# Kernel optimization log

Measured on AMD Instinct MI355X. Metric: run time of the kernel, lower is better.

The kernel has to match this reference:

```python
import jax, jax.numpy as jnp
import numpy as np

DIM = 2048
HEADS = 32
WINDOW = 8   # local_attn
B = 4
N = 197


def _local_mask(w, n):
    # Faithful to local_attention(): for row i, columns j in [max(i-w,0), min(i+w, n))
    # get weight (w - |i-j|/2)/w; everything else is 0 (later masked to -inf).
    i = jnp.arange(n)[:, None]
    j = jnp.arange(n)[None, :]
    d = jnp.abs(i - j).astype(jnp.float32)
    in_win = (j >= i - w) & (j < i + w)  # range(start, end) excludes i+w
    return jnp.where(in_win, (w - d / 2.0) / w, 0.0)  # (N, N)


def setup_inputs() -> dict:
    key = jax.random.key(0)
    k1, k2, k3, k4 = jax.random.split(key, 4)
    x = jax.random.normal(k1, (B, N, DIM), dtype=jnp.float32)
    qkv_w = jax.random.normal(k2, (3 * DIM, DIM), dtype=jnp.float32) * 0.02  # no qkv bias
    proj_w = jax.random.normal(k3, (DIM, DIM), dtype=jnp.float32) * 0.02
    proj_b = jax.random.normal(k4, (DIM,), dtype=jnp.float32) * 0.02
    return {"x": x, "qkv_w": qkv_w, "proj_w": proj_w, "proj_b": proj_b}


def reference(x, qkv_w, proj_w, proj_b):
    Bb, Nn, C = x.shape
    H = HEADS
    hd = C // H
    scale = hd ** (-0.5)
    # qkv projection: (B, N, 3C) -> (3, B, H, N, hd)
    qkv = (x @ qkv_w.T).reshape(Bb, Nn, 3, H, hd).transpose(2, 0, 3, 1, 4)
    q, k, v = qkv[0], qkv[1], qkv[2]
    attn = jnp.einsum('bhnd,bhmd->bhnm', q, k) * scale  # (B, H, N, N)
    m = _local_mask(WINDOW, Nn)  # (N, N), broadcasts over B, H
    # attn * mask, then masked_fill(mask == 0, -inf), then softmax
    attn = jnp.where(m != 0.0, attn * m, -jnp.inf)
    attn = jax.nn.softmax(attn, axis=-1)
    out = jnp.einsum('bhnm,bhmd->bhnd', attn, v)  # (B, H, N, hd)
    out = out.transpose(0, 2, 1, 3).reshape(Bb, Nn, C)
    return out @ proj_w.T + proj_b
```

## Files before the change

kernel.cpp:

```cpp
#include <hip/hip_runtime.h>
#include <math.h>

#define B_SZ   4
#define N_SEQ  197
#define DIMC   2048
#define HEADS  32
#define HD     64
#define WIN    8
#define M_ROWS (B_SZ * N_SEQ)
#define M_PAD  896

using f32x4 = __attribute__((ext_vector_type(4))) float;
using s16x8 = __attribute__((ext_vector_type(8))) short;

__device__ inline ushort f2bf(float f) {
  uint x = __float_as_uint(f);
  uint r = (x + 0x7fffu + ((x >> 16) & 1u)) >> 16;
  return (ushort)r;
}
__device__ inline float bf2f(ushort u) {
  return __uint_as_float(((uint)u) << 16);
}

__device__ inline void gload16(const ushort* g, ushort* l) {
  __builtin_amdgcn_global_load_lds(
      (const __attribute__((address_space(1))) unsigned int*)g,
      (__attribute__((address_space(3))) unsigned int*)l, 16, 0, 0);
}

#define NX (M_ROWS * DIMC / 8)
#define NQ (3 * DIMC * DIMC / 8)
#define NP (DIMC * DIMC / 8)

__global__ __launch_bounds__(256)
void cvt_all(const float* __restrict__ x,  const float* __restrict__ qw,
             const float* __restrict__ pw, ushort* __restrict__ xb,
             ushort* __restrict__ qwb, ushort* __restrict__ pwb) {
  int i = blockIdx.x * 256 + threadIdx.x;
  const float* src; ushort* dst; int idx;
  if (i < NX)                { src = x;  dst = xb;  idx = i; }
  else if (i < NX + NQ)      { src = qw; dst = qwb; idx = i - NX; }
  else if (i < NX + NQ + NP) { src = pw; dst = pwb; idx = i - NX - NQ; }
  else return;
  f32x4 a = ((const f32x4*)src)[2 * idx];
  f32x4 b = ((const f32x4*)src)[2 * idx + 1];
  ushort4 u0, u1;
  u0.x = f2bf(a.x); u0.y = f2bf(a.y); u0.z = f2bf(a.z); u0.w = f2bf(a.w);
  u1.x = f2bf(b.x); u1.y = f2bf(b.y); u1.z = f2bf(b.z); u1.w = f2bf(b.w);
  ((ushort4*)dst)[2 * idx]     = u0;
  ((ushort4*)dst)[2 * idx + 1] = u1;
}

__global__ __launch_bounds__(256, 3)
void gemm_bt_bf16(const ushort* __restrict__ A, const ushort* __restrict__ Bw,
                  ushort* __restrict__ Cout,
                  int Mdim, int Ndim, int Kfull, int Ksplit) {
  __shared__ ushort As[3][128 * 32];
  __shared__ ushort Bs[3][128 * 32];
  const int tid  = threadIdx.x;
  const int lane = tid & 63;
  const int wave = tid >> 6;

  const int nwg  = gridDim.x * gridDim.y;
  const int phys = blockIdx.y * gridDim.x + blockIdx.x;
  const int cpx  = nwg >> 3;
  const int lg   = (phys & 7) * cpx + (phys >> 3);
  const int m0 = (lg % gridDim.x) * 128;
  const int n0 = (lg / gridDim.x) * 128;
  const int koff = blockIdx.z * Ksplit;
  ushort* C = Cout + (size_t)blockIdx.z * Mdim * Ndim;

  const int wr = (wave >> 1) * 64;
  const int wc = (wave & 1) * 64;
  const int fr = lane & 15;
  const int kg = lane >> 4;
  const int srow = lane >> 2;
  const int scol = ((lane & 3) ^ ((srow >> 1) & 3)) * 8;
  const int rdA  = (kg ^ ((fr >> 1) & 3)) * 8;

  f32x4 acc[4][4];
#pragma unroll
  for (int i = 0; i < 4; ++i)
#pragma unroll
    for (int j = 0; j < 4; ++j)
      acc[i][j] = (f32x4){0.f, 0.f, 0.f, 0.f};

  const ushort* Asrc0 = A  + (size_t)(m0 + wave * 32 + srow)      * Kfull + koff + scol;
  const ushort* Asrc1 = A  + (size_t)(m0 + wave * 32 + 16 + srow) * Kfull + koff + scol;
  const ushort* Bsrc0 = Bw + (size_t)(n0 + wave * 32 + srow)      * Kfull + koff + scol;
  const ushort* Bsrc1 = Bw + (size_t)(n0 + wave * 32 + 16 + srow) * Kfull + koff + scol;

  const int nt = Ksplit >> 5;

  auto STAGE = [&](int kk, int b) {
    const int k = kk << 5;
    gload16(Asrc0 + k, &As[b][wave * 1024]);
    gload16(Asrc1 + k, &As[b][wave * 1024 + 512]);
    gload16(Bsrc0 + k, &Bs[b][wave * 1024]);
    gload16(Bsrc1 + k, &Bs[b][wave * 1024 + 512]);
  };

  STAGE(0, 0);
  STAGE(1, 1);

  int cur = 0, s2 = 2;
  for (int t = 0; t < nt; ++t) {
    if (t < nt - 1) asm volatile("s_waitcnt vmcnt(4)" ::: "memory");
    else            asm volatile("s_waitcnt vmcnt(0)" ::: "memory");
    __builtin_amdgcn_s_barrier();
    __builtin_amdgcn_sched_barrier(0);

    if (t + 2 < nt) STAGE(t + 2, s2);

    s16x8 af[4], bfr[4];
#pragma unroll
    for (int i = 0; i < 4; ++i)
      af[i] = *(const s16x8*)(&As[cur][(wr + i * 16 + fr) * 32 + rdA]);
#pragma unroll
    for (int j = 0; j < 4; ++j)
      bfr[j] = *(const s16x8*)(&Bs[cur][(wc + j * 16 + fr) * 32 + rdA]);
    __builtin_amdgcn_s_setprio(1);
#pragma unroll
    for (int i = 0; i < 4; ++i)
#pragma unroll
      for (int j = 0; j < 4; ++j)
        acc[i][j] = __builtin_amdgcn_mfma_f32_16x16x32_bf16(af[i], bfr[j], acc[i][j], 0, 0, 0);
    __builtin_amdgcn_s_setprio(0);

    cur += 1; if (cur >= 3) cur -= 3;
    s2  += 1; if (s2  >= 3) s2  -= 3;
  }

  const int crow_base = m0 + wr + kg * 4;
  const int ccol_base = n0 + wc + fr;
#pragma unroll
  for (int j = 0; j < 4; ++j) {
    int col = ccol_base + j * 16;
#pragma unroll
    for (int i = 0; i < 4; ++i)
#pragma unroll
      for (int r = 0; r < 4; ++r) {
        int grow = crow_base + i * 16 + r;
        if (grow < Mdim) C[(size_t)grow * Ndim + col] = f2bf(acc[i][j][r]);
      }
  }
}

__global__ __launch_bounds__(256)
void local_attn(const ushort* __restrict__ p0, const ushort* __restrict__ p1,
                ushort* __restrict__ ao) {
  __shared__ float plds[4][16][68];
  const int wv = threadIdx.x >> 6;
  const int gw = blockIdx.x * 4 + wv;
  if (gw >= B_SZ * HEADS * N_SEQ) return;
  const int lane = threadIdx.x & 63;
  const int jj = lane >> 2;
  const int ds = lane & 3;
  const int h = gw % HEADS;
  const int t = gw / HEADS;
  const int i = t % N_SEQ;
  const int b = t / N_SEQ;
  const int row = b * N_SEQ + i;
  const size_t stride = 3 * DIMC;

  int j0 = i - WIN; if (j0 < 0) j0 = 0;
  int j1 = i + WIN; if (j1 > N_SEQ) j1 = N_SEQ;
  const int j = j0 + jj;
  const bool ok = (j < j1);
  const int jc = ok ? j : (j1 - 1);

  float qs[16];
  {
    const size_t qi = (size_t)row * stride + h * HD + ds * 16;
    s16x8 a0 = *(const s16x8*)(p0 + qi);
    s16x8 a1 = *(const s16x8*)(p0 + qi + 8);
    s16x8 b0 = *(const s16x8*)(p1 + qi);
    s16x8 b1 = *(const s16x8*)(p1 + qi + 8);
#pragma unroll
    for (int e = 0; e < 8; ++e) {
      qs[e]     = (bf2f((ushort)a0[e]) + bf2f((ushort)b0[e])) * 0.125f;
      qs[8 + e] = (bf2f((ushort)a1[e]) + bf2f((ushort)b1[e])) * 0.125f;
    }
  }

  float s;
  {
    const size_t ki = (size_t)(b * N_SEQ + jc) * stride + DIMC + h * HD + ds * 16;
    s16x8 a0 = *(const s16x8*)(p0 + ki);
    s16x8 a1 = *(const s16x8*)(p0 + ki + 8);
    s16x8 b0 = *(const s16x8*)(p1 + ki);
    s16x8 b1 = *(const s16x8*)(p1 + ki + 8);
    float acc = 0.f;
#pragma unroll
    for (int e = 0; e < 8; ++e) {
      acc += qs[e]     * (bf2f((ushort)a0[e]) + bf2f((ushort)b0[e]));
      acc += qs[8 + e] * (bf2f((ushort)a1[e]) + bf2f((ushort)b1[e]));
    }
    s = acc;
  }
  s += __shfl_xor(s, 1);
  s += __shfl_xor(s, 2);

  {
    float d = fabsf((float)(i - j));
    float m = 1.0f - d * 0.0625f;
    s = ok ? s * m : -INFINITY;
  }

  float mx = s;
  mx = fmaxf(mx, __shfl_xor(mx, 4));
  mx = fmaxf(mx, __shfl_xor(mx, 8));
  mx = fmaxf(mx, __shfl_xor(mx, 16));
  mx = fmaxf(mx, __shfl_xor(mx, 32));
  float e = __expf(s - mx);
  float sum = e;
  sum += __shfl_xor(sum, 4);
  sum += __shfl_xor(sum, 8);
  sum += __shfl_xor(sum, 16);
  sum += __shfl_xor(sum, 32);
  const float inv = 1.f / sum;

  {
    const size_t vi = (size_t)(b * N_SEQ + jc) * stride + 2 * DIMC + h * HD + ds * 16;
    s16x8 a0 = *(const s16x8*)(p0 + vi);
    s16x8 a1 = *(const s16x8*)(p0 + vi + 8);
    s16x8 b0 = *(const s16x8*)(p1 + vi);
    s16x8 b1 = *(const s16x8*)(p1 + vi + 8);
    const float ee = ok ? e : 0.f;
    f32x4 w0, w1, w2, w3;
#pragma unroll
    for (int g = 0; g < 4; ++g) {
      w0[g] = ee * (bf2f((ushort)a0[g])     + bf2f((ushort)b0[g]));
      w1[g] = ee * (bf2f((ushort)a0[4 + g]) + bf2f((ushort)b0[4 + g]));
      w2[g] = ee * (bf2f((ushort)a1[g])     + bf2f((ushort)b1[g]));
      w3[g] = ee * (bf2f((ushort)a1[4 + g]) + bf2f((ushort)b1[4 + g]));
    }
    *(f32x4*)&plds[wv][jj][ds * 16]      = w0;
    *(f32x4*)&plds[wv][jj][ds * 16 + 4]  = w1;
    *(f32x4*)&plds[wv][jj][ds * 16 + 8]  = w2;
    *(f32x4*)&plds[wv][jj][ds * 16 + 12] = w3;
  }
  asm volatile("s_waitcnt lgkmcnt(0)" ::: "memory");
  __builtin_amdgcn_sched_barrier(0);

  float o = 0.f;
#pragma unroll
  for (int q = 0; q < 16; ++q) o += plds[wv][q][lane];
  ao[(size_t)row * DIMC + h * HD + lane] = f2bf(o * inv);
}

#define NR8 (M_ROWS * DIMC / 8)
__global__ __launch_bounds__(256)
void reduce4_bias(const ushort* __restrict__ parts, const float* __restrict__ bias,
                  float* __restrict__ out) {
  int i = blockIdx.x * 256 + threadIdx.x;
  if (i >= NR8) return;
  const size_t slice = (size_t)M_ROWS * DIMC;
  float a[8];
#pragma unroll
  for (int e = 0; e < 8; ++e) a[e] = 0.f;
#pragma unroll
  for (int z = 0; z < 4; ++z) {
    s16x8 v = *(const s16x8*)(parts + z * slice + (size_t)i * 8);
#pragma unroll
    for (int e = 0; e < 8; ++e) a[e] += bf2f((ushort)v[e]);
  }
  const int col = (i * 8) & (DIMC - 1);
  f32x4 b0 = *(const f32x4*)(bias + col);
  f32x4 b1 = *(const f32x4*)(bias + col + 4);
  f32x4 o0 = {a[0] + b0.x, a[1] + b0.y, a[2] + b0.z, a[3] + b0.w};
  f32x4 o1 = {a[4] + b1.x, a[5] + b1.y, a[6] + b1.z, a[7] + b1.w};
  ((f32x4*)out)[2 * i]     = o0;
  ((f32x4*)out)[2 * i + 1] = o1;
}

extern "C" void kernel_launch(void* const* d_in, const int* in_sizes, int n_in,
                              void* d_out, int out_size, void* d_ws, size_t ws_size,
                              hipStream_t stream) {
  const float* x      = (const float*)d_in[0];
  const float* qkv_w  = (const float*)d_in[1];
  const float* proj_w = (const float*)d_in[2];
  const float* proj_b = (const float*)d_in[3];
  float* out = (float*)d_out;

  char* p = (char*)d_ws;
  ushort* x_bf    = (ushort*)p;  p += (size_t)M_PAD * DIMC * 2;
  ushort* qkvw_bf = (ushort*)p;  p += (size_t)3 * DIMC * DIMC * 2;
  ushort* projw_bf= (ushort*)p;  p += (size_t)DIMC * DIMC * 2;
  ushort* qkv_p   = (ushort*)p;  p += (size_t)2 * M_ROWS * 3 * DIMC * 2;
  ushort* ao_bf   = (ushort*)p;  p += (size_t)M_PAD * DIMC * 2;
  ushort* proj_p  = (ushort*)p;

  dim3 blk(256);

  {
    int total = NX + NQ + NP;
    cvt_all<<<dim3((total + 255) / 256), blk, 0, stream>>>(
        x, qkv_w, proj_w, x_bf, qkvw_bf, projw_bf);
  }

  gemm_bt_bf16<<<dim3(M_PAD / 128, (3 * DIMC) / 128, 2), blk, 0, stream>>>(
      x_bf, qkvw_bf, qkv_p, M_ROWS, 3 * DIMC, DIMC, DIMC / 2);

  int total_waves = B_SZ * HEADS * N_SEQ;
  local_attn<<<dim3((total_waves + 3) / 4), blk, 0, stream>>>(
      qkv_p, qkv_p + (size_t)M_ROWS * 3 * DIMC, ao_bf);

  gemm_bt_bf16<<<dim3(M_PAD / 128, DIMC / 128, 4), blk, 0, stream>>>(
      ao_bf, projw_bf, proj_p, M_ROWS, DIMC, DIMC, DIMC / 4);

  reduce4_bias<<<dim3((NR8 + 255) / 256), blk, 0, stream>>>(proj_p, proj_b, out);
}
```

Baseline: 86.90 us.

## Stage K/V per head chunk in LDS and halve proj GEMM split-K

The local attention kernel now assigns one block per (batch, head, half-sequence) and first stages that chunk's K and V rows, already summed from the two split-K partials and converted to fp32, into shared memory. Each query row then reads K/V from LDS instead of reloading its 16-row window from global memory. This cuts redundant global traffic by roughly the window size, at the cost of only 256 blocks and a serial loop of queries per wave. The projection GEMM also drops from 4-way to 2-way split-K, which halves the partial buffers the reduce kernel reads but gives the GEMM fewer blocks.

```diff
diff --git a/kernel.cpp b/kernel.cpp
--- a/kernel.cpp
+++ b/kernel.cpp
@@ -146,112 +146,139 @@
   }
 }
 
-__global__ __launch_bounds__(256)
+#define NRW   106
+#define NGR   (NRW * 8)
+__global__ __launch_bounds__(512)
 void local_attn(const ushort* __restrict__ p0, const ushort* __restrict__ p1,
                 ushort* __restrict__ ao) {
-  __shared__ float plds[4][16][68];
-  const int wv = threadIdx.x >> 6;
-  const int gw = blockIdx.x * 4 + wv;
-  if (gw >= B_SZ * HEADS * N_SEQ) return;
+  __shared__ float kl[NRW * 68];
+  __shared__ float vl[NRW * 68];
+  __shared__ float plds[8][16][68];
+  const int bh    = blockIdx.x >> 1;
+  const int chunk = blockIdx.x & 1;
+  const int b = bh >> 5;
+  const int h = bh & 31;
+  const int c0     = chunk ? 99 : 0;
+  const int ch_len = chunk ? 98 : 99;
+  const int r0     = chunk ? 91 : 0;
+  const size_t stride = 3 * DIMC;
+
+  for (int g = threadIdx.x; g < 2 * NGR; g += 512) {
+    const int isv = (g >= NGR);
+    const int gg  = isv ? g - NGR : g;
+    const int r   = gg >> 3;
+    const int seg = gg & 7;
+    const size_t src = (size_t)(b * N_SEQ + r0 + r) * stride
+                     + (isv ? 2 : 1) * DIMC + h * HD + seg * 8;
+    s16x8 a = *(const s16x8*)(p0 + src);
+    s16x8 c = *(const s16x8*)(p1 + src);
+    float* dst = (isv ? vl : kl) + r * 68 + seg * 8;
+    if (isv) {
+#pragma unroll
+      for (int e = 0; e < 8; ++e) dst[e] = bf2f((ushort)a[e]) + bf2f((ushort)c[e]);
+    } else {
+#pragma unroll
+      for (int e = 0; e < 8; ++e) dst[e] = (bf2f((ushort)a[e]) + bf2f((ushort)c[e])) * 0.125f;
+    }
+  }
+  __syncthreads();
+
+  const int wv   = threadIdx.x >> 6;
   const int lane = threadIdx.x & 63;
-  const int jj = lane >> 2;
-  const int ds = lane & 3;
-  const int h = gw % HEADS;
-  const int t = gw / HEADS;
-  const int i = t % N_SEQ;
-  const int b = t / N_SEQ;
-  const int row = b * N_SEQ + i;
-  const size_t stride = 3 * DIMC;
-
-  int j0 = i - WIN; if (j0 < 0) j0 = 0;
-  int j1 = i + WIN; if (j1 > N_SEQ) j1 = N_SEQ;
-  const int j = j0 + jj;
-  const bool ok = (j < j1);
-  const int jc = ok ? j : (j1 - 1);
-
-  float qs[16];
-  {
-    const size_t qi = (size_t)row * stride + h * HD + ds * 16;
-    s16x8 a0 = *(const s16x8*)(p0 + qi);
-    s16x8 a1 = *(const s16x8*)(p0 + qi + 8);
-    s16x8 b0 = *(const s16x8*)(p1 + qi);
-    s16x8 b1 = *(const s16x8*)(p1 + qi + 8);
-#pragma unroll
-    for (int e = 0; e < 8; ++e) {
-      qs[e]     = (bf2f((ushort)a0[e]) + bf2f((ushort)b0[e])) * 0.125f;
-      qs[8 + e] = (bf2f((ushort)a1[e]) + bf2f((ushort)b1[e])) * 0.125f;
-    }
-  }
-
-  float s;
-  {
-    const size_t ki = (size_t)(b * N_SEQ + jc) * stride + DIMC + h * HD + ds * 16;
-    s16x8 a0 = *(const s16x8*)(p0 + ki);
-    s16x8 a1 = *(const s16x8*)(p0 + ki + 8);
-    s16x8 b0 = *(const s16x8*)(p1 + ki);
-    s16x8 b1 = *(const s16x8*)(p1 + ki + 8);
-    float acc = 0.f;
-#pragma unroll
-    for (int e = 0; e < 8; ++e) {
-      acc += qs[e]     * (bf2f((ushort)a0[e]) + bf2f((ushort)b0[e]));
-      acc += qs[8 + e] * (bf2f((ushort)a1[e]) + bf2f((ushort)b1[e]));
-    }
-    s = acc;
-  }
-  s += __shfl_xor(s, 1);
-  s += __shfl_xor(s, 2);
-
-  {
-    float d = fabsf((float)(i - j));
-    float m = 1.0f - d * 0.0625f;
-    s = ok ? s * m : -INFINITY;
-  }
-
-  float mx = s;
-  mx = fmaxf(mx, __shfl_xor(mx, 4));
-  mx = fmaxf(mx, __shfl_xor(mx, 8));
-  mx = fmaxf(mx, __shfl_xor(mx, 16));
-  mx = fmaxf(mx, __shfl_xor(mx, 32));
-  float e = __expf(s - mx);
-  float sum = e;
-  sum += __shfl_xor(sum, 4);
-  sum += __shfl_xor(sum, 8);
-  sum += __shfl_xor(sum, 16);
-  sum += __shfl_xor(sum, 32);
-  const float inv = 1.f / sum;
-
-  {
-    const size_t vi = (size_t)(b * N_SEQ + jc) * stride + 2 * DIMC + h * HD + ds * 16;
-    s16x8 a0 = *(const s16x8*)(p0 + vi);
-    s16x8 a1 = *(const s16x8*)(p0 + vi + 8);
-    s16x8 b0 = *(const s16x8*)(p1 + vi);
-    s16x8 b1 = *(const s16x8*)(p1 + vi + 8);
-    const float ee = ok ? e : 0.f;
-    f32x4 w0, w1, w2, w3;
-#pragma unroll
-    for (int g = 0; g < 4; ++g) {
-      w0[g] = ee * (bf2f((ushort)a0[g])     + bf2f((ushort)b0[g]));
-      w1[g] = ee * (bf2f((ushort)a0[4 + g]) + bf2f((ushort)b0[4 + g]));
-      w2[g] = ee * (bf2f((ushort)a1[g])     + bf2f((ushort)b1[g]));
-      w3[g] = ee * (bf2f((ushort)a1[4 + g]) + bf2f((ushort)b1[4 + g]));
-    }
-    *(f32x4*)&plds[wv][jj][ds * 16]      = w0;
-    *(f32x4*)&plds[wv][jj][ds * 16 + 4]  = w1;
-    *(f32x4*)&plds[wv][jj][ds * 16 + 8]  = w2;
-    *(f32x4*)&plds[wv][jj][ds * 16 + 12] = w3;
-  }
-  asm volatile("s_waitcnt lgkmcnt(0)" ::: "memory");
-  __builtin_amdgcn_sched_barrier(0);
-
-  float o = 0.f;
-#pragma unroll
-  for (int q = 0; q < 16; ++q) o += plds[wv][q][lane];
-  ao[(size_t)row * DIMC + h * HD + lane] = f2bf(o * inv);
+  const int jj   = lane >> 2;
+  const int ds   = lane & 3;
+
+  for (int ii = wv; ii < ch_len; ii += 8) {
+    const int i = c0 + ii;
+    int j0 = i - WIN; if (j0 < 0) j0 = 0;
+    int j1 = i + WIN; if (j1 > N_SEQ) j1 = N_SEQ;
+    const int j = j0 + jj;
+    const bool ok = (j < j1);
+    const int jc = ok ? j : (j1 - 1);
+    const int lr = jc - r0;
+
+    float qs[16];
+    {
+      const size_t qi = (size_t)(b * N_SEQ + i) * stride + h * HD + ds * 16;
+      s16x8 a0 = *(const s16x8*)(p0 + qi);
+      s16x8 a1 = *(const s16x8*)(p0 + qi + 8);
+      s16x8 b0 = *(const s16x8*)(p1 + qi);
+      s16x8 b1 = *(const s16x8*)(p1 + qi + 8);
+#pragma unroll
+      for (int e = 0; e < 8; ++e) {
+        qs[e]     = bf2f((ushort)a0[e]) + bf2f((ushort)b0[e]);
+        qs[8 + e] = bf2f((ushort)a1[e]) + bf2f((ushort)b1[e]);
+      }
+    }
+
+    float s = 0.f;
+    {
+      const float* kr = kl + lr * 68 + ds * 16;
+      f32x4 k0 = *(const f32x4*)(kr);
+      f32x4 k1 = *(const f32x4*)(kr + 4);
+      f32x4 k2 = *(const f32x4*)(kr + 8);
+      f32x4 k3 = *(const f32x4*)(kr + 12);
+#pragma unroll
+      for (int e = 0; e < 4; ++e) {
+        s += qs[e]      * k0[e];
+        s += qs[4 + e]  * k1[e];
+        s += qs[8 + e]  * k2[e];
+        s += qs[12 + e] * k3[e];
+      }
+    }
+    s += __shfl_xor(s, 1);
+    s += __shfl_xor(s, 2);
+
+    {
+      float d = fabsf((float)(i - j));
+      float m = 1.0f - d * 0.0625f;
+      s = ok ? s * m : -INFINITY;
+    }
+
+    float mx = s;
+    mx = fmaxf(mx, __shfl_xor(mx, 4));
+    mx = fmaxf(mx, __shfl_xor(mx, 8));
+    mx = fmaxf(mx, __shfl_xor(mx, 16));
+    mx = fmaxf(mx, __shfl_xor(mx, 32));
+    float e = __expf(s - mx);
+    float sum = e;
+    sum += __shfl_xor(sum, 4);
+    sum += __shfl_xor(sum, 8);
+    sum += __shfl_xor(sum, 16);
+    sum += __shfl_xor(sum, 32);
+    const float inv = 1.f / sum;
+
+    {
+      const float* vr = vl + lr * 68 + ds * 16;
+      const float ee = ok ? e : 0.f;
+      f32x4 v0 = *(const f32x4*)(vr);
+      f32x4 v1 = *(const f32x4*)(vr + 4);
+      f32x4 v2 = *(const f32x4*)(vr + 8);
+      f32x4 v3 = *(const f32x4*)(vr + 12);
+      f32x4 w0, w1, w2, w3;
+#pragma unroll
+      for (int g = 0; g < 4; ++g) {
+        w0[g] = ee * v0[g]; w1[g] = ee * v1[g];
+        w2[g] = ee * v2[g]; w3[g] = ee * v3[g];
+      }
+      *(f32x4*)&plds[wv][jj][ds * 16]      = w0;
+      *(f32x4*)&plds[wv][jj][ds * 16 + 4]  = w1;
+      *(f32x4*)&plds[wv][jj][ds * 16 + 8]  = w2;
+      *(f32x4*)&plds[wv][jj][ds * 16 + 12] = w3;
+    }
+    asm volatile("s_waitcnt lgkmcnt(0)" ::: "memory");
+    __builtin_amdgcn_sched_barrier(0);
+
+    float o = 0.f;
+#pragma unroll
+    for (int q = 0; q < 16; ++q) o += plds[wv][q][lane];
+    ao[(size_t)(b * N_SEQ + i) * DIMC + h * HD + lane] = f2bf(o * inv);
+  }
 }
 
 #define NR8 (M_ROWS * DIMC / 8)
 __global__ __launch_bounds__(256)
-void reduce4_bias(const ushort* __restrict__ parts, const float* __restrict__ bias,
+void reduce2_bias(const ushort* __restrict__ parts, const float* __restrict__ bias,
                   float* __restrict__ out) {
   int i = blockIdx.x * 256 + threadIdx.x;
   if (i >= NR8) return;
@@ -260,7 +287,7 @@
 #pragma unroll
   for (int e = 0; e < 8; ++e) a[e] = 0.f;
 #pragma unroll
-  for (int z = 0; z < 4; ++z) {
+  for (int z = 0; z < 2; ++z) {
     s16x8 v = *(const s16x8*)(parts + z * slice + (size_t)i * 8);
 #pragma unroll
     for (int e = 0; e < 8; ++e) a[e] += bf2f((ushort)v[e]);
@@ -302,12 +329,11 @@
   gemm_bt_bf16<<<dim3(M_PAD / 128, (3 * DIMC) / 128, 2), blk, 0, stream>>>(
       x_bf, qkvw_bf, qkv_p, M_ROWS, 3 * DIMC, DIMC, DIMC / 2);
 
-  int total_waves = B_SZ * HEADS * N_SEQ;
-  local_attn<<<dim3((total_waves + 3) / 4), blk, 0, stream>>>(
+  local_attn<<<dim3(B_SZ * HEADS * 2), dim3(512), 0, stream>>>(
       qkv_p, qkv_p + (size_t)M_ROWS * 3 * DIMC, ao_bf);
 
-  gemm_bt_bf16<<<dim3(M_PAD / 128, DIMC / 128, 4), blk, 0, stream>>>(
-      ao_bf, projw_bf, proj_p, M_ROWS, DIMC, DIMC, DIMC / 4);
-
-  reduce4_bias<<<dim3((NR8 + 255) / 256), blk, 0, stream>>>(proj_p, proj_b, out);
-}
+  gemm_bt_bf16<<<dim3(M_PAD / 128, DIMC / 128, 2), blk, 0, stream>>>(
+      ao_bf, projw_bf, proj_p, M_ROWS, DIMC, DIMC, DIMC / 2);
+
+  reduce2_bias<<<dim3((NR8 + 255) / 256), blk, 0, stream>>>(proj_p, proj_b, out);
+}
```

New measurement: 96.25 us. 10.8% more time.

## Replace split-K partial buffers and reduce kernel with fp32 atomic accumulation

Applied to the files above, without the earlier changes.

The GEMMs no longer write bf16 split-K partial slices. They now atomically add fp32 results into buffers that the conversion kernel zero-fills first, and the bias is folded into the z==0 slice of the projection GEMM. This removes the separate reduce kernel and the partial-sum traffic, and the attention kernel now reads fp32 qkv directly instead of summing two bf16 partials. The projection split-K drops from 4 to 2. Atomics are scattered scalar ops with possible contention, the summation order becomes nondeterministic, and the zero-fill adds extra writes.

```diff
diff --git a/kernel.cpp b/kernel.cpp
--- a/kernel.cpp
+++ b/kernel.cpp
@@ -28,20 +28,33 @@
       (__attribute__((address_space(3))) unsigned int*)l, 16, 0, 0);
 }
 
-#define NX (M_ROWS * DIMC / 8)
-#define NQ (3 * DIMC * DIMC / 8)
-#define NP (DIMC * DIMC / 8)
+#define NX  (M_ROWS * DIMC / 8)
+#define NQ  (3 * DIMC * DIMC / 8)
+#define NP  (DIMC * DIMC / 8)
+#define NZQ (M_ROWS * 3 * DIMC / 8)
+#define NZO (M_ROWS * DIMC / 8)
 
 __global__ __launch_bounds__(256)
 void cvt_all(const float* __restrict__ x,  const float* __restrict__ qw,
              const float* __restrict__ pw, ushort* __restrict__ xb,
-             ushort* __restrict__ qwb, ushort* __restrict__ pwb) {
+             ushort* __restrict__ qwb, ushort* __restrict__ pwb,
+             float* __restrict__ qkvz, float* __restrict__ outz) {
   int i = blockIdx.x * 256 + threadIdx.x;
   const float* src; ushort* dst; int idx;
   if (i < NX)                { src = x;  dst = xb;  idx = i; }
   else if (i < NX + NQ)      { src = qw; dst = qwb; idx = i - NX; }
   else if (i < NX + NQ + NP) { src = pw; dst = pwb; idx = i - NX - NQ; }
-  else return;
+  else if (i < NX + NQ + NP + NZQ) {
+    int z = i - NX - NQ - NP;
+    ((f32x4*)qkvz)[2 * z]     = (f32x4){0.f, 0.f, 0.f, 0.f};
+    ((f32x4*)qkvz)[2 * z + 1] = (f32x4){0.f, 0.f, 0.f, 0.f};
+    return;
+  } else if (i < NX + NQ + NP + NZQ + NZO) {
+    int z = i - NX - NQ - NP - NZQ;
+    ((f32x4*)outz)[2 * z]     = (f32x4){0.f, 0.f, 0.f, 0.f};
+    ((f32x4*)outz)[2 * z + 1] = (f32x4){0.f, 0.f, 0.f, 0.f};
+    return;
+  } else return;
   f32x4 a = ((const f32x4*)src)[2 * idx];
   f32x4 b = ((const f32x4*)src)[2 * idx + 1];
   ushort4 u0, u1;
@@ -52,9 +65,9 @@
 }
 
 __global__ __launch_bounds__(256, 3)
-void gemm_bt_bf16(const ushort* __restrict__ A, const ushort* __restrict__ Bw,
-                  ushort* __restrict__ Cout,
-                  int Mdim, int Ndim, int Kfull, int Ksplit) {
+void gemm_bt_atomic(const ushort* __restrict__ A, const ushort* __restrict__ Bw,
+                    float* __restrict__ C, const float* __restrict__ bias,
+                    int Mdim, int Ndim, int Kfull, int Ksplit) {
   __shared__ ushort As[3][128 * 32];
   __shared__ ushort Bs[3][128 * 32];
   const int tid  = threadIdx.x;
@@ -68,7 +81,6 @@
   const int m0 = (lg % gridDim.x) * 128;
   const int n0 = (lg / gridDim.x) * 128;
   const int koff = blockIdx.z * Ksplit;
-  ushort* C = Cout + (size_t)blockIdx.z * Mdim * Ndim;
 
   const int wr = (wave >> 1) * 64;
   const int wc = (wave & 1) * 64;
@@ -133,22 +145,23 @@
 
   const int crow_base = m0 + wr + kg * 4;
   const int ccol_base = n0 + wc + fr;
+  const bool addb = (bias != nullptr) && (blockIdx.z == 0);
 #pragma unroll
   for (int j = 0; j < 4; ++j) {
     int col = ccol_base + j * 16;
+    float bv = addb ? bias[col] : 0.f;
 #pragma unroll
     for (int i = 0; i < 4; ++i)
 #pragma unroll
       for (int r = 0; r < 4; ++r) {
         int grow = crow_base + i * 16 + r;
-        if (grow < Mdim) C[(size_t)grow * Ndim + col] = f2bf(acc[i][j][r]);
+        if (grow < Mdim) atomicAdd(&C[(size_t)grow * Ndim + col], acc[i][j][r] + bv);
       }
   }
 }
 
 __global__ __launch_bounds__(256)
-void local_attn(const ushort* __restrict__ p0, const ushort* __restrict__ p1,
-                ushort* __restrict__ ao) {
+void local_attn(const float* __restrict__ qkv, ushort* __restrict__ ao) {
   __shared__ float plds[4][16][68];
   const int wv = threadIdx.x >> 6;
   const int gw = blockIdx.x * 4 + wv;
@@ -169,34 +182,33 @@
   const bool ok = (j < j1);
   const int jc = ok ? j : (j1 - 1);
 
-  float qs[16];
-  {
-    const size_t qi = (size_t)row * stride + h * HD + ds * 16;
-    s16x8 a0 = *(const s16x8*)(p0 + qi);
-    s16x8 a1 = *(const s16x8*)(p0 + qi + 8);
-    s16x8 b0 = *(const s16x8*)(p1 + qi);
-    s16x8 b1 = *(const s16x8*)(p1 + qi + 8);
-#pragma unroll
-    for (int e = 0; e < 8; ++e) {
-      qs[e]     = (bf2f((ushort)a0[e]) + bf2f((ushort)b0[e])) * 0.125f;
-      qs[8 + e] = (bf2f((ushort)a1[e]) + bf2f((ushort)b1[e])) * 0.125f;
+  f32x4 q0, q1, q2, q3;
+  {
+    const float* qp = qkv + (size_t)row * stride + h * HD + ds * 16;
+    q0 = *(const f32x4*)(qp);
+    q1 = *(const f32x4*)(qp + 4);
+    q2 = *(const f32x4*)(qp + 8);
+    q3 = *(const f32x4*)(qp + 12);
+#pragma unroll
+    for (int e = 0; e < 4; ++e) {
+      q0[e] *= 0.125f; q1[e] *= 0.125f; q2[e] *= 0.125f; q3[e] *= 0.125f;
     }
   }
 
-  float s;
-  {
-    const size_t ki = (size_t)(b * N_SEQ + jc) * stride + DIMC + h * HD + ds * 16;
-    s16x8 a0 = *(const s16x8*)(p0 + ki);
-    s16x8 a1 = *(const s16x8*)(p0 + ki + 8);
-    s16x8 b0 = *(const s16x8*)(p1 + ki);
-    s16x8 b1 = *(const s16x8*)(p1 + ki + 8);
-    float acc = 0.f;
-#pragma unroll
-    for (int e = 0; e < 8; ++e) {
-      acc += qs[e]     * (bf2f((ushort)a0[e]) + bf2f((ushort)b0[e]));
-      acc += qs[8 + e] * (bf2f((ushort)a1[e]) + bf2f((ushort)b1[e]));
+  float s = 0.f;
+  {
+    const float* kp = qkv + (size_t)(b * N_SEQ + jc) * stride + DIMC + h * HD + ds * 16;
+    f32x4 k0 = *(const f32x4*)(kp);
+    f32x4 k1 = *(const f32x4*)(kp + 4);
+    f32x4 k2 = *(const f32x4*)(kp + 8);
+    f32x4 k3 = *(const f32x4*)(kp + 12);
+#pragma unroll
+    for (int e = 0; e < 4; ++e) {
+      s += q0[e] * k0[e];
+      s += q1[e] * k1[e];
+      s += q2[e] * k2[e];
+      s += q3[e] * k3[e];
     }
-    s = acc;
   }
   s += __shfl_xor(s, 1);
   s += __shfl_xor(s, 2);
@@ -221,19 +233,17 @@
   const float inv = 1.f / sum;
 
   {
-    const size_t vi = (size_t)(b * N_SEQ + jc) * stride + 2 * DIMC + h * HD + ds * 16;
-    s16x8 a0 = *(const s16x8*)(p0 + vi);
-    s16x8 a1 = *(const s16x8*)(p0 + vi + 8);
-    s16x8 b0 = *(const s16x8*)(p1 + vi);
-    s16x8 b1 = *(const s16x8*)(p1 + vi + 8);
+    const float* vp = qkv + (size_t)(b * N_SEQ + jc) * stride + 2 * DIMC + h * HD + ds * 16;
+    f32x4 v0 = *(const f32x4*)(vp);
+    f32x4 v1 = *(const f32x4*)(vp + 4);
+    f32x4 v2 = *(const f32x4*)(vp + 8);
+    f32x4 v3 = *(const f32x4*)(vp + 12);
     const float ee = ok ? e : 0.f;
     f32x4 w0, w1, w2, w3;
 #pragma unroll
     for (int g = 0; g < 4; ++g) {
-      w0[g] = ee * (bf2f((ushort)a0[g])     + bf2f((ushort)b0[g]));
-      w1[g] = ee * (bf2f((ushort)a0[4 + g]) + bf2f((ushort)b0[4 + g]));
-      w2[g] = ee * (bf2f((ushort)a1[g])     + bf2f((ushort)b1[g]));
-      w3[g] = ee * (bf2f((ushort)a1[4 + g]) + bf2f((ushort)b1[4 + g]));
+      w0[g] = ee * v0[g]; w1[g] = ee * v1[g];
+      w2[g] = ee * v2[g]; w3[g] = ee * v3[g];
     }
     *(f32x4*)&plds[wv][jj][ds * 16]      = w0;
     *(f32x4*)&plds[wv][jj][ds * 16 + 4]  = w1;
@@ -247,31 +257,6 @@
 #pragma unroll
   for (int q = 0; q < 16; ++q) o += plds[wv][q][lane];
   ao[(size_t)row * DIMC + h * HD + lane] = f2bf(o * inv);
-}
-
-#define NR8 (M_ROWS * DIMC / 8)
-__global__ __launch_bounds__(256)
-void reduce4_bias(const ushort* __restrict__ parts, const float* __restrict__ bias,
-                  float* __restrict__ out) {
-  int i = blockIdx.x * 256 + threadIdx.x;
-  if (i >= NR8) return;
-  const size_t slice = (size_t)M_ROWS * DIMC;
-  float a[8];
-#pragma unroll
-  for (int e = 0; e < 8; ++e) a[e] = 0.f;
-#pragma unroll
-  for (int z = 0; z < 4; ++z) {
-    s16x8 v = *(const s16x8*)(parts + z * slice + (size_t)i * 8);
-#pragma unroll
-    for (int e = 0; e < 8; ++e) a[e] += bf2f((ushort)v[e]);
-  }
-  const int col = (i * 8) & (DIMC - 1);
-  f32x4 b0 = *(const f32x4*)(bias + col);
-  f32x4 b1 = *(const f32x4*)(bias + col + 4);
-  f32x4 o0 = {a[0] + b0.x, a[1] + b0.y, a[2] + b0.z, a[3] + b0.w};
-  f32x4 o1 = {a[4] + b1.x, a[5] + b1.y, a[6] + b1.z, a[7] + b1.w};
-  ((f32x4*)out)[2 * i]     = o0;
-  ((f32x4*)out)[2 * i + 1] = o1;
 }
 
 extern "C" void kernel_launch(void* const* d_in, const int* in_sizes, int n_in,
@@ -287,27 +272,23 @@
   ushort* x_bf    = (ushort*)p;  p += (size_t)M_PAD * DIMC * 2;
   ushort* qkvw_bf = (ushort*)p;  p += (size_t)3 * DIMC * DIMC * 2;
   ushort* projw_bf= (ushort*)p;  p += (size_t)DIMC * DIMC * 2;
-  ushort* qkv_p   = (ushort*)p;  p += (size_t)2 * M_ROWS * 3 * DIMC * 2;
-  ushort* ao_bf   = (ushort*)p;  p += (size_t)M_PAD * DIMC * 2;
-  ushort* proj_p  = (ushort*)p;
+  float*  qkv_f   = (float*)p;   p += (size_t)M_ROWS * 3 * DIMC * 4;
+  ushort* ao_bf   = (ushort*)p;
 
   dim3 blk(256);
 
   {
-    int total = NX + NQ + NP;
+    int total = NX + NQ + NP + NZQ + NZO;
     cvt_all<<<dim3((total + 255) / 256), blk, 0, stream>>>(
-        x, qkv_w, proj_w, x_bf, qkvw_bf, projw_bf);
-  }
-
-  gemm_bt_bf16<<<dim3(M_PAD / 128, (3 * DIMC) / 128, 2), blk, 0, stream>>>(
-      x_bf, qkvw_bf, qkv_p, M_ROWS, 3 * DIMC, DIMC, DIMC / 2);
+        x, qkv_w, proj_w, x_bf, qkvw_bf, projw_bf, qkv_f, out);
+  }
+
+  gemm_bt_atomic<<<dim3(M_PAD / 128, (3 * DIMC) / 128, 2), blk, 0, stream>>>(
+      x_bf, qkvw_bf, qkv_f, nullptr, M_ROWS, 3 * DIMC, DIMC, DIMC / 2);
 
   int total_waves = B_SZ * HEADS * N_SEQ;
-  local_attn<<<dim3((total_waves + 3) / 4), blk, 0, stream>>>(
-      qkv_p, qkv_p + (size_t)M_ROWS * 3 * DIMC, ao_bf);
-
-  gemm_bt_bf16<<<dim3(M_PAD / 128, DIMC / 128, 4), blk, 0, stream>>>(
-      ao_bf, projw_bf, proj_p, M_ROWS, DIMC, DIMC, DIMC / 4);
-
-  reduce4_bias<<<dim3((NR8 + 255) / 256), blk, 0, stream>>>(proj_p, proj_b, out);
-}
+  local_attn<<<dim3((total_waves + 3) / 4), blk, 0, stream>>>(qkv_f, ao_bf);
+
+  gemm_bt_atomic<<<dim3(M_PAD / 128, DIMC / 128, 2), blk, 0, stream>>>(
+      ao_bf, projw_bf, out, proj_b, M_ROWS, DIMC, DIMC, DIMC / 2);
+}
```

New measurement: 138.0 us. 1.59x slower.

## Pre-reduce QKV split-K partials into head-major layout; halve proj split-K

Applied to the files above, without the earlier changes.

Adds a kernel that sums the two split-K partial QKV outputs and writes them in a per-tensor, per-head, row-major layout. The attention kernel then reads one contiguous buffer per Q/K/V instead of two strided partial buffers, which cuts redundant loads and adds across the overlapping windows. Separately, the output projection's split-K factor drops from 4 to 2, and the final reduction now sums two partials instead of four. The cost is an extra kernel launch plus an extra QKV-sized write and read. Q and K are also each rounded to bf16 once more before the dot product.

```diff
diff --git a/kernel.cpp b/kernel.cpp
--- a/kernel.cpp
+++ b/kernel.cpp
@@ -146,9 +146,29 @@
   }
 }
 
+#define NGQ (M_ROWS * 3 * DIMC / 8)
 __global__ __launch_bounds__(256)
-void local_attn(const ushort* __restrict__ p0, const ushort* __restrict__ p1,
-                ushort* __restrict__ ao) {
+void reduce_qkv_t(const ushort* __restrict__ p0, const ushort* __restrict__ p1,
+                  ushort* __restrict__ qt) {
+  int i = blockIdx.x * 256 + threadIdx.x;
+  if (i >= NGQ) return;
+  const int row = i / 768;
+  const int c8  = i - row * 768;
+  const int col = c8 * 8;
+  const int tns = col >> 11;
+  const int h   = (col >> 6) & 31;
+  const int d   = col & 63;
+  s16x8 a = *(const s16x8*)(p0 + (size_t)i * 8);
+  s16x8 b = *(const s16x8*)(p1 + (size_t)i * 8);
+  s16x8 r;
+#pragma unroll
+  for (int e = 0; e < 8; ++e)
+    r[e] = (short)f2bf(bf2f((ushort)a[e]) + bf2f((ushort)b[e]));
+  *(s16x8*)(qt + ((size_t)(tns * HEADS + h) * M_ROWS + row) * HD + d) = r;
+}
+
+__global__ __launch_bounds__(256)
+void local_attn(const ushort* __restrict__ qt, ushort* __restrict__ ao) {
   __shared__ float plds[4][16][68];
   const int wv = threadIdx.x >> 6;
   const int gw = blockIdx.x * 4 + wv;
@@ -161,42 +181,40 @@
   const int i = t % N_SEQ;
   const int b = t / N_SEQ;
   const int row = b * N_SEQ + i;
-  const size_t stride = 3 * DIMC;
+
+  const ushort* qb = qt + (size_t)h * M_ROWS * HD;
+  const ushort* kb = qt + (size_t)(HEADS + h) * M_ROWS * HD;
+  const ushort* vb = qt + (size_t)(2 * HEADS + h) * M_ROWS * HD;
 
   int j0 = i - WIN; if (j0 < 0) j0 = 0;
   int j1 = i + WIN; if (j1 > N_SEQ) j1 = N_SEQ;
   const int j = j0 + jj;
   const bool ok = (j < j1);
   const int jc = ok ? j : (j1 - 1);
+  const int krow = b * N_SEQ + jc;
 
   float qs[16];
   {
-    const size_t qi = (size_t)row * stride + h * HD + ds * 16;
-    s16x8 a0 = *(const s16x8*)(p0 + qi);
-    s16x8 a1 = *(const s16x8*)(p0 + qi + 8);
-    s16x8 b0 = *(const s16x8*)(p1 + qi);
-    s16x8 b1 = *(const s16x8*)(p1 + qi + 8);
+    const ushort* qp = qb + (size_t)row * HD + ds * 16;
+    s16x8 a0 = *(const s16x8*)(qp);
+    s16x8 a1 = *(const s16x8*)(qp + 8);
 #pragma unroll
     for (int e = 0; e < 8; ++e) {
-      qs[e]     = (bf2f((ushort)a0[e]) + bf2f((ushort)b0[e])) * 0.125f;
-      qs[8 + e] = (bf2f((ushort)a1[e]) + bf2f((ushort)b1[e])) * 0.125f;
+      qs[e]     = bf2f((ushort)a0[e]);
+      qs[8 + e] = bf2f((ushort)a1[e]);
     }
   }
 
-  float s;
-  {
-    const size_t ki = (size_t)(b * N_SEQ + jc) * stride + DIMC + h * HD + ds * 16;
-    s16x8 a0 = *(const s16x8*)(p0 + ki);
-    s16x8 a1 = *(const s16x8*)(p0 + ki + 8);
-    s16x8 b0 = *(const s16x8*)(p1 + ki);
-    s16x8 b1 = *(const s16x8*)(p1 + ki + 8);
-    float acc = 0.f;
+  float s = 0.f;
+  {
+    const ushort* kp = kb + (size_t)krow * HD + ds * 16;
+    s16x8 a0 = *(const s16x8*)(kp);
+    s16x8 a1 = *(const s16x8*)(kp + 8);
 #pragma unroll
     for (int e = 0; e < 8; ++e) {
-      acc += qs[e]     * (bf2f((ushort)a0[e]) + bf2f((ushort)b0[e]));
-      acc += qs[8 + e] * (bf2f((ushort)a1[e]) + bf2f((ushort)b1[e]));
+      s += qs[e]     * bf2f((ushort)a0[e]);
+      s += qs[8 + e] * bf2f((ushort)a1[e]);
     }
-    s = acc;
   }
   s += __shfl_xor(s, 1);
   s += __shfl_xor(s, 2);
@@ -204,7 +222,7 @@
   {
     float d = fabsf((float)(i - j));
     float m = 1.0f - d * 0.0625f;
-    s = ok ? s * m : -INFINITY;
+    s = ok ? s * 0.125f * m : -INFINITY;
   }
 
   float mx = s;
@@ -221,19 +239,17 @@
   const float inv = 1.f / sum;
 
   {
-    const size_t vi = (size_t)(b * N_SEQ + jc) * stride + 2 * DIMC + h * HD + ds * 16;
-    s16x8 a0 = *(const s16x8*)(p0 + vi);
-    s16x8 a1 = *(const s16x8*)(p0 + vi + 8);
-    s16x8 b0 = *(const s16x8*)(p1 + vi);
-    s16x8 b1 = *(const s16x8*)(p1 + vi + 8);
+    const ushort* vp = vb + (size_t)krow * HD + ds * 16;
+    s16x8 a0 = *(const s16x8*)(vp);
+    s16x8 a1 = *(const s16x8*)(vp + 8);
     const float ee = ok ? e : 0.f;
     f32x4 w0, w1, w2, w3;
 #pragma unroll
     for (int g = 0; g < 4; ++g) {
-      w0[g] = ee * (bf2f((ushort)a0[g])     + bf2f((ushort)b0[g]));
-      w1[g] = ee * (bf2f((ushort)a0[4 + g]) + bf2f((ushort)b0[4 + g]));
-      w2[g] = ee * (bf2f((ushort)a1[g])     + bf2f((ushort)b1[g]));
-      w3[g] = ee * (bf2f((ushort)a1[4 + g]) + bf2f((ushort)b1[4 + g]));
+      w0[g] = ee * bf2f((ushort)a0[g]);
+      w1[g] = ee * bf2f((ushort)a0[4 + g]);
+      w2[g] = ee * bf2f((ushort)a1[g]);
+      w3[g] = ee * bf2f((ushort)a1[4 + g]);
     }
     *(f32x4*)&plds[wv][jj][ds * 16]      = w0;
     *(f32x4*)&plds[wv][jj][ds * 16 + 4]  = w1;
@@ -251,7 +267,7 @@
 
 #define NR8 (M_ROWS * DIMC / 8)
 __global__ __launch_bounds__(256)
-void reduce4_bias(const ushort* __restrict__ parts, const float* __restrict__ bias,
+void reduce2_bias(const ushort* __restrict__ parts, const float* __restrict__ bias,
                   float* __restrict__ out) {
   int i = blockIdx.x * 256 + threadIdx.x;
   if (i >= NR8) return;
@@ -260,7 +276,7 @@
 #pragma unroll
   for (int e = 0; e < 8; ++e) a[e] = 0.f;
 #pragma unroll
-  for (int z = 0; z < 4; ++z) {
+  for (int z = 0; z < 2; ++z) {
     s16x8 v = *(const s16x8*)(parts + z * slice + (size_t)i * 8);
 #pragma unroll
     for (int e = 0; e < 8; ++e) a[e] += bf2f((ushort)v[e]);
@@ -288,6 +304,7 @@
   ushort* qkvw_bf = (ushort*)p;  p += (size_t)3 * DIMC * DIMC * 2;
   ushort* projw_bf= (ushort*)p;  p += (size_t)DIMC * DIMC * 2;
   ushort* qkv_p   = (ushort*)p;  p += (size_t)2 * M_ROWS * 3 * DIMC * 2;
+  ushort* qkv_t   = (ushort*)p;  p += (size_t)M_ROWS * 3 * DIMC * 2;
   ushort* ao_bf   = (ushort*)p;  p += (size_t)M_PAD * DIMC * 2;
   ushort* proj_p  = (ushort*)p;
 
@@ -302,12 +319,14 @@
   gemm_bt_bf16<<<dim3(M_PAD / 128, (3 * DIMC) / 128, 2), blk, 0, stream>>>(
       x_bf, qkvw_bf, qkv_p, M_ROWS, 3 * DIMC, DIMC, DIMC / 2);
 
+  reduce_qkv_t<<<dim3((NGQ + 255) / 256), blk, 0, stream>>>(
+      qkv_p, qkv_p + (size_t)M_ROWS * 3 * DIMC, qkv_t);
+
   int total_waves = B_SZ * HEADS * N_SEQ;
-  local_attn<<<dim3((total_waves + 3) / 4), blk, 0, stream>>>(
-      qkv_p, qkv_p + (size_t)M_ROWS * 3 * DIMC, ao_bf);
-
-  gemm_bt_bf16<<<dim3(M_PAD / 128, DIMC / 128, 4), blk, 0, stream>>>(
-      ao_bf, projw_bf, proj_p, M_ROWS, DIMC, DIMC, DIMC / 4);
-
-  reduce4_bias<<<dim3((NR8 + 255) / 256), blk, 0, stream>>>(proj_p, proj_b, out);
-}
+  local_attn<<<dim3((total_waves + 3) / 4), blk, 0, stream>>>(qkv_t, ao_bf);
+
+  gemm_bt_bf16<<<dim3(M_PAD / 128, DIMC / 128, 2), blk, 0, stream>>>(
+      ao_bf, projw_bf, proj_p, M_ROWS, DIMC, DIMC, DIMC / 2);
+
+  reduce2_bias<<<dim3((NR8 + 255) / 256), blk, 0, stream>>>(proj_p, proj_b, out);
+}
```

Result: slower. 93.52 us (+7.6%).
